# Performance work log

Measured on AMD Instinct MI355X. Metric: run time of the kernel, lower is better.

## Reference

```python
import jax, jax.numpy as jnp
import numpy as np

HEADS1, HID1 = 4, 64   # layer 1: concat -> 256
HEADS2, HID2 = 1, 64   # layer 2: out_channels
NEG_SLOPE = 0.2


def gat_layer(x_src, x_dst, W_src, W_dst, att_src, att_dst, bias, src, dst, n_tgt, heads, hid):
    # bipartite GATConv (PyG math), concat heads
    xs = (x_src @ W_src).reshape(-1, heads, hid)          # [Ns,H,C]
    xd = (x_dst @ W_dst).reshape(-1, heads, hid)          # [Nt,H,C]
    a_s = jnp.sum(xs * att_src, axis=-1)                  # [Ns,H]
    a_d = jnp.sum(xd * att_dst, axis=-1)                  # [Nt,H]
    e = jax.nn.leaky_relu(a_s[src] + a_d[dst], NEG_SLOPE) # [E,H]
    m = jax.ops.segment_max(e, dst, num_segments=n_tgt)
    m = jnp.where(jnp.isfinite(m), m, 0.0)
    ex = jnp.exp(e - m[dst])
    denom = jax.ops.segment_sum(ex, dst, num_segments=n_tgt)
    alpha = ex / (denom[dst] + 1e-16)                     # edge softmax per target
    msg = xs[src] * alpha[:, :, None]                     # [E,H,C]
    out = jax.ops.segment_sum(msg, dst, num_segments=n_tgt)
    return out.reshape(n_tgt, heads * hid) + bias


def setup_inputs() -> dict:
    key = jax.random.key(0)
    ks = jax.random.split(key, 20)
    N0, NT1, NT2 = 100000, 25000, 5000
    E1, E2 = 400000, 100000
    IN, H1 = 256, HEADS1 * HID1  # 256
    OUT = HEADS2 * HID2          # 64
    g = lambda k, sh, fan: jax.random.normal(k, sh, jnp.float32) * (1.0 / np.sqrt(fan))
    return {
        'x': jax.random.normal(ks[0], (N0, IN), jnp.float32),
        'src1': jax.random.randint(ks[1], (E1,), 0, N0),
        'dst1': jax.random.randint(ks[2], (E1,), 0, NT1),
        'src2': jax.random.randint(ks[3], (E2,), 0, NT1),
        'dst2': jax.random.randint(ks[4], (E2,), 0, NT2),
        'n_tgt1': NT1, 'n_tgt2': NT2,
        'W1_src': g(ks[5], (IN, H1), IN), 'W1_dst': g(ks[6], (IN, H1), IN),
        'att1_src': g(ks[7], (HEADS1, HID1), HID1), 'att1_dst': g(ks[8], (HEADS1, HID1), HID1),
        'bias1': jnp.zeros((H1,), jnp.float32),
        'skip1_W': g(ks[9], (IN, H1), IN), 'skip1_b': jnp.zeros((H1,), jnp.float32),
        'W2_src': g(ks[10], (H1, OUT), H1), 'W2_dst': g(ks[11], (H1, OUT), H1),
        'att2_src': g(ks[12], (HEADS2, HID2), HID2), 'att2_dst': g(ks[13], (HEADS2, HID2), HID2),
        'bias2': jnp.zeros((OUT,), jnp.float32),
        'skip2_W': g(ks[14], (H1, OUT), H1), 'skip2_b': jnp.zeros((OUT,), jnp.float32),
    }


def reference(x, src1, dst1, src2, dst2, n_tgt1, n_tgt2,
              W1_src, W1_dst, att1_src, att1_dst, bias1, skip1_W, skip1_b,
              W2_src, W2_dst, att2_src, att2_dst, bias2, skip2_W, skip2_b):
    # layer 1: conv + skip + elu (dropout inactive in eval)
    x_t1 = x[:n_tgt1]
    h = gat_layer(x, x_t1, W1_src, W1_dst, att1_src, att1_dst, bias1,
                  src1, dst1, n_tgt1, HEADS1, HID1)
    h = h + (x_t1 @ skip1_W + skip1_b)
    h = jax.nn.elu(h)
    # layer 2 (final): conv + skip, then log_softmax
    x_t2 = h[:n_tgt2]
    o = gat_layer(h, x_t2, W2_src, W2_dst, att2_src, att2_dst, bias2,
                  src2, dst2, n_tgt2, HEADS2, HID2)
    o = o + (x_t2 @ skip2_W + skip2_b)
    return jax.nn.log_softmax(o, axis=-1)
```

## Files before the change

kernel.cpp:

```cpp
#include <hip/hip_runtime.h>
#include <hip/hip_bf16.h>

using bf16 = __hip_bfloat16;
typedef __attribute__((ext_vector_type(8))) short short8;
typedef __attribute__((ext_vector_type(4))) short short4v;
typedef __attribute__((ext_vector_type(4))) float float4v;

__device__ __forceinline__ short f2bs(float x) {
    bf16 b = __float2bfloat16(x);
    return __builtin_bit_cast(short, b);
}
__device__ __forceinline__ float bs2f(short s) {
    return __uint_as_float(((unsigned)(unsigned short)s) << 16);
}
__device__ __forceinline__ void glds16(const void* g, void* l) {
    __builtin_amdgcn_global_load_lds(
        (const __attribute__((address_space(1))) unsigned int*)g,
        (__attribute__((address_space(3))) unsigned int*)l, 16, 0, 0);
}

__global__ __launch_bounds__(512, 4) void gemm_l1(
        const float* __restrict__ A, const bf16* __restrict__ Bt,
        bf16* __restrict__ xs1, bf16* __restrict__ sk1,
        float* __restrict__ as1, float* __restrict__ ad1,
        const float* __restrict__ att_s, const float* __restrict__ att_d,
        int M, int NT) {
    __shared__ short ldsB[2][32 * 512];
    const int row0 = blockIdx.x * 128;
    const int tid = threadIdx.x;
    const int wave = tid >> 6, lane = tid & 63;
    const int quad = lane >> 4, l16 = lane & 15;

    auto stageB = [&](int y, int buf) {
#pragma unroll
        for (int i = 0; i < 4; i++) {
            int blk = wave * 4 + i;
            int cb = blk >> 3, kit = blk & 7;
            glds16(&Bt[(size_t)(y * 64 + cb * 16 + l16) * 256 + kit * 32 + quad * 8],
                   &ldsB[buf][blk * 512]);
        }
    };

    stageB(0, 0);

    const int arow_ = row0 + wave * 16 + l16;
    const int arow = arow_ < M ? arow_ : M - 1;
    const float* Ap = &A[(size_t)arow * 256 + quad * 8];
    short8 afr[8];
#pragma unroll
    for (int half = 0; half < 2; half++) {
        float4v r0[4], r1[4];
#pragma unroll
        for (int k = 0; k < 4; k++) {
            r0[k] = *(const float4v*)(Ap + (half * 4 + k) * 32);
            r1[k] = *(const float4v*)(Ap + (half * 4 + k) * 32 + 4);
        }
#pragma unroll
        for (int k = 0; k < 4; k++) {
            short8 v;
#pragma unroll
            for (int j = 0; j < 4; j++) { v[j] = f2bs(r0[k][j]); v[4 + j] = f2bs(r1[k][j]); }
            afr[half * 4 + k] = v;
        }
    }

    const int ymax = row0 < NT ? 12 : 4;
    const int rbase = row0 + wave * 16 + quad * 4;

    __syncthreads();

    for (int y = 0; y < ymax; y++) {
        const int cur = y & 1;
        if (y + 1 < ymax) stageB(y + 1, cur ^ 1);

        const float4v fz = {0.f, 0.f, 0.f, 0.f};
        float4v acc[4];
#pragma unroll
        for (int n = 0; n < 4; n++) acc[n] = fz;
#pragma unroll
        for (int kit = 0; kit < 8; kit++)
#pragma unroll
            for (int n = 0; n < 4; n++) {
                short8 bf = *(short8*)&ldsB[cur][(n * 8 + kit) * 512 + lane * 8];
                acc[n] = __builtin_amdgcn_mfma_f32_16x16x32_bf16(afr[kit], bf, acc[n], 0, 0, 0);
            }

        if (y < 8) {
            const float* attc = y < 4 ? att_s : att_d;
            const int head = y & 3;
            const int aM = y < 4 ? M : NT;
            float* aout = y < 4 ? as1 : ad1;
            float av[4];
#pragma unroll
            for (int n = 0; n < 4; n++) av[n] = attc[head * 64 + n * 16 + l16];
#pragma unroll
            for (int r = 0; r < 4; r++) {
                float t = acc[0][r] * av[0] + acc[1][r] * av[1] +
                          acc[2][r] * av[2] + acc[3][r] * av[3];
                t += __shfl_xor(t, 1, 64);
                t += __shfl_xor(t, 2, 64);
                t += __shfl_xor(t, 4, 64);
                t += __shfl_xor(t, 8, 64);
                int grow = rbase + r;
                if (l16 == 0 && grow < aM) aout[(size_t)grow * 4 + head] = t;
            }
        }
        if (y < 4) {
#pragma unroll
            for (int n = 0; n < 4; n++) {
                int col = y * 64 + n * 16 + l16;
#pragma unroll
                for (int r = 0; r < 4; r++) {
                    int row = rbase + r;
                    if (row < M) xs1[(size_t)row * 256 + col] = __float2bfloat16(acc[n][r]);
                }
            }
        } else if (y >= 8) {
#pragma unroll
            for (int n = 0; n < 4; n++) {
                int scol = (y - 8) * 64 + n * 16 + l16;
#pragma unroll
                for (int r = 0; r < 4; r++) {
                    int row = rbase + r;
                    if (row < NT) sk1[(size_t)row * 256 + scol] = __float2bfloat16(acc[n][r]);
                }
            }
        }
        __syncthreads();
    }
}

__global__ __launch_bounds__(512, 4) void gemm_l2(
        const bf16* __restrict__ Ah, const bf16* __restrict__ Bt,
        float* __restrict__ x2, float* __restrict__ a2,
        const float* __restrict__ attc, int NT) {
    __shared__ short ldsB[32 * 512];
    const int y = blockIdx.y;
    const int row0 = blockIdx.x * 128;
    const int col0 = y * 64;
    const int tid = threadIdx.x;
    const int wave = tid >> 6, lane = tid & 63;
    const int quad = lane >> 4, l16 = lane & 15;

#pragma unroll
    for (int i = 0; i < 4; i++) {
        int blk = wave * 4 + i;
        int cb = blk >> 3, kit = blk & 7;
        glds16(&Bt[(size_t)(col0 + cb * 16 + l16) * 256 + kit * 32 + quad * 8],
               &ldsB[blk * 512]);
    }

    const int arow = row0 + wave * 16 + l16;
    const bf16* Ap = &Ah[(size_t)arow * 256 + quad * 8];

    short8 s[8];
#pragma unroll
    for (int kit = 0; kit < 8; kit++) s[kit] = *(const short8*)(Ap + kit * 32);

    const float4v fz = {0.f, 0.f, 0.f, 0.f};
    float4v acc[4];
#pragma unroll
    for (int n = 0; n < 4; n++) acc[n] = fz;

    __syncthreads();

#pragma unroll
    for (int kit = 0; kit < 8; kit++) {
#pragma unroll
        for (int n = 0; n < 4; n++) {
            short8 bf = *(short8*)&ldsB[(n * 8 + kit) * 512 + lane * 8];
            acc[n] = __builtin_amdgcn_mfma_f32_16x16x32_bf16(s[kit], bf, acc[n], 0, 0, 0);
        }
    }

    const int rbase = row0 + wave * 16 + quad * 4;

    if (y < 2) {
        float av[4];
#pragma unroll
        for (int n = 0; n < 4; n++) av[n] = attc[y * 64 + n * 16 + l16];
#pragma unroll
        for (int r = 0; r < 4; r++) {
            float t = acc[0][r] * av[0] + acc[1][r] * av[1] +
                      acc[2][r] * av[2] + acc[3][r] * av[3];
            t += __shfl_xor(t, 1, 64);
            t += __shfl_xor(t, 2, 64);
            t += __shfl_xor(t, 4, 64);
            t += __shfl_xor(t, 8, 64);
            int grow = rbase + r;
            if (l16 == 0 && grow < NT) a2[(size_t)grow * 2 + y] = t;
        }
    }
#pragma unroll
    for (int n = 0; n < 4; n++) {
        int col = col0 + n * 16 + l16;
#pragma unroll
        for (int r = 0; r < 4; r++) {
            int row = rbase + r;
            if (row < NT) x2[(size_t)row * 192 + col] = acc[n][r];
        }
    }
}

__global__ void prep_s(
        const int* __restrict__ s1, const int* __restrict__ d1, int E1,
        const int* __restrict__ s2, const int* __restrict__ d2, int E2,
        int* __restrict__ fill1, int* __restrict__ fill2,
        int* __restrict__ psrc1, int* __restrict__ psrc2,
        const float* __restrict__ W1s, const float* __restrict__ W1d,
        const float* __restrict__ W1sk, const float* __restrict__ W2s,
        const float* __restrict__ W2d, const float* __restrict__ W2sk,
        const float* __restrict__ a2s, const float* __restrict__ a2d,
        bf16* __restrict__ Wt1, bf16* __restrict__ Wt2,
        float* __restrict__ at2c) {
    int t = blockIdx.x * blockDim.x + threadIdx.x;
    if (t < E1) {
        int d = d1[t];
        int pos = atomicAdd(&fill1[d], 1);
        if (pos < 64) psrc1[(d << 6) + pos] = s1[t];
        return;
    }
    t -= E1;
    if (t < E2) {
        int d = d2[t];
        int pos = atomicAdd(&fill2[d], 1);
        if (pos < 64) psrc2[(d << 6) + pos] = s2[t];
        return;
    }
    t -= E2;
    if (t < 196608) {
        int n = t >> 8, k = t & 255;
        const float* W = n < 256 ? W1s : (n < 512 ? W1d : W1sk);
        Wt1[t] = __float2bfloat16(W[k * 256 + (n & 255)]);
    } else if (t < 245760) {
        int i = t - 196608;
        int n = i >> 8, k = i & 255;
        const float* W = n < 64 ? W2s : (n < 128 ? W2d : W2sk);
        Wt2[i] = __float2bfloat16(W[k * 64 + (n & 63)]);
    } else if (t < 245888) {
        int i = t - 245760;
        at2c[i] = i < 64 ? a2s[i] : a2d[i - 64];
    }
}

__global__ __launch_bounds__(256) void agg_h4(
        const int* __restrict__ fill, const int* __restrict__ psrc,
        const bf16* __restrict__ X, const float* __restrict__ as1,
        const float* __restrict__ ad1, const float* __restrict__ bias,
        const bf16* __restrict__ skip, const float* __restrict__ skipb,
        bf16* __restrict__ h) {
    __shared__ float exl[4][64][4];
    __shared__ float red[4][256];
    const int d = blockIdx.x;
    const int tid = threadIdx.x;
    const int wv = tid >> 6, lane = tid & 63;
    const int head = lane >> 4;
    int deg = fill[d];
    deg = deg < 64 ? deg : 64;
    int se = 0;
    float4v ex4 = {0.f, 0.f, 0.f, 0.f};
    const float4v ad4 = *(const float4v*)&ad1[(size_t)d * 4];
    if (lane < deg) {
        se = psrc[((size_t)d << 6) + lane];
        float4v as4 = *(const float4v*)&as1[(size_t)se * 4];
#pragma unroll
        for (int c = 0; c < 4; c++) {
            float v = as4[c] + ad4[c];
            v = v > 0.f ? v : 0.2f * v;
            ex4[c] = expf(v);
        }
    }
    *(float4v*)&exl[wv][lane][0] = ex4;
    float4v dn = ex4;
#pragma unroll
    for (int o = 32; o; o >>= 1) {
        dn.x += __shfl_xor(dn.x, o, 64);
        dn.y += __shfl_xor(dn.y, o, 64);
        dn.z += __shfl_xor(dn.z, o, 64);
        dn.w += __shfl_xor(dn.w, o, 64);
    }
    float4v acc = {0.f, 0.f, 0.f, 0.f}, acc2 = {0.f, 0.f, 0.f, 0.f};
    int p = wv;
    for (; p + 4 < deg; p += 8) {
        int sA = __shfl(se, p, 64), sB = __shfl(se, p + 4, 64);
        float aA = exl[wv][p][head], aB = exl[wv][p + 4][head];
        short4v xa = *(const short4v*)&X[(size_t)sA * 256 + lane * 4];
        short4v xb = *(const short4v*)&X[(size_t)sB * 256 + lane * 4];
        acc.x += bs2f(xa.x) * aA; acc2.x += bs2f(xb.x) * aB;
        acc.y += bs2f(xa.y) * aA; acc2.y += bs2f(xb.y) * aB;
        acc.z += bs2f(xa.z) * aA; acc2.z += bs2f(xb.z) * aB;
        acc.w += bs2f(xa.w) * aA; acc2.w += bs2f(xb.w) * aB;
    }
    for (; p < deg; p += 4) {
        int sA = __shfl(se, p, 64);
        float aA = exl[wv][p][head];
        short4v xa = *(const short4v*)&X[(size_t)sA * 256 + lane * 4];
        acc.x += bs2f(xa.x) * aA;
        acc.y += bs2f(xa.y) * aA;
        acc.z += bs2f(xa.z) * aA;
        acc.w += bs2f(xa.w) * aA;
    }
    acc.x += acc2.x; acc.y += acc2.y; acc.z += acc2.z; acc.w += acc2.w;
    *(float4v*)&red[wv][lane * 4] = acc;
    __syncthreads();
    const int f = tid;
    float sum = red[0][f] + red[1][f] + red[2][f] + red[3][f];
    int hf = f >> 6;
    float den = hf == 0 ? dn.x : hf == 1 ? dn.y : hf == 2 ? dn.z : dn.w;
    float v = sum / (den + 1e-16f) + bias[f] + __bfloat162float(skip[(size_t)d * 256 + f]) +
              skipb[f];
    h[(size_t)d * 256 + f] = __float2bfloat16(v > 0.f ? v : expm1f(v));
}

__global__ __launch_bounds__(256) void agg_h1(
        const int* __restrict__ fill2, const int* __restrict__ psrc2,
        const float* __restrict__ x2, const float* __restrict__ a2,
        const float* __restrict__ bias, const float* __restrict__ skipb,
        float* __restrict__ out, int M) {
    const int d = blockIdx.x * 4 + (threadIdx.x >> 6);
    const int lane = threadIdx.x & 63;
    if (d >= M) return;
    int deg = fill2[d];
    deg = deg < 64 ? deg : 64;
    int se = 0;
    float exv = 0.f;
    const float adv = a2[(size_t)d * 2 + 1];
    if (lane < deg) {
        se = psrc2[((size_t)d << 6) + lane];
        float v = a2[(size_t)se * 2] + adv;
        v = v > 0.f ? v : 0.2f * v;
        exv = expf(v);
    }
    float den = exv;
#pragma unroll
    for (int o = 32; o; o >>= 1) den += __shfl_xor(den, o, 64);
    float acc = 0.f, acc2 = 0.f;
    int p = 0;
    for (; p + 1 < deg; p += 2) {
        int sA = __shfl(se, p, 64), sB = __shfl(se, p + 1, 64);
        float aA = __shfl(exv, p, 64), aB = __shfl(exv, p + 1, 64);
        acc += x2[(size_t)sA * 192 + lane] * aA;
        acc2 += x2[(size_t)sB * 192 + lane] * aB;
    }
    if (p < deg) {
        int sA = __shfl(se, p, 64);
        acc += x2[(size_t)sA * 192 + lane] * __shfl(exv, p, 64);
    }
    float v = (acc + acc2) / (den + 1e-16f) + bias[lane] +
              x2[(size_t)d * 192 + 128 + lane] + skipb[lane];
    float m = v;
#pragma unroll
    for (int o = 32; o; o >>= 1) m = fmaxf(m, __shfl_xor(m, o, 64));
    float e = expf(v - m);
#pragma unroll
    for (int o = 32; o; o >>= 1) e += __shfl_xor(e, o, 64);
    out[(size_t)d * 64 + lane] = v - m - logf(e);
}

extern "C" void kernel_launch(void* const* d_in, const int* in_sizes, int n_in,
                              void* d_out, int out_size, void* d_ws, size_t ws_size,
                              hipStream_t stream) {
    const float* x        = (const float*)d_in[0];
    const int*   src1     = (const int*)d_in[1];
    const int*   dst1     = (const int*)d_in[2];
    const int*   src2     = (const int*)d_in[3];
    const int*   dst2     = (const int*)d_in[4];
    const float* W1_src   = (const float*)d_in[7];
    const float* W1_dst   = (const float*)d_in[8];
    const float* att1_src = (const float*)d_in[9];
    const float* att1_dst = (const float*)d_in[10];
    const float* bias1    = (const float*)d_in[11];
    const float* skip1_W  = (const float*)d_in[12];
    const float* skip1_b  = (const float*)d_in[13];
    const float* W2_src   = (const float*)d_in[14];
    const float* W2_dst   = (const float*)d_in[15];
    const float* att2_src = (const float*)d_in[16];
    const float* att2_dst = (const float*)d_in[17];
    const float* bias2    = (const float*)d_in[18];
    const float* skip2_b  = (const float*)d_in[20];
    const float* skip2_W  = (const float*)d_in[19];

    const int N0  = in_sizes[0] / 256;
    const int E1  = in_sizes[1];
    const int E2  = in_sizes[3];
    const int NT1 = 25000, NT2 = 5000;
    const int NT1p = 25088;

    char* ws = (char*)d_ws;
    size_t off = 0;
    auto alloc = [&](size_t b) { size_t o = off; off += (b + 255) & ~(size_t)255; return o; };
    size_t o_xs1   = alloc((size_t)N0 * 256 * 2);
    size_t o_sk1   = alloc((size_t)NT1 * 256 * 2);
    size_t o_h     = alloc((size_t)NT1p * 256 * 2);
    size_t o_as1   = alloc((size_t)N0 * 4 * 4);
    size_t o_ad1   = alloc((size_t)NT1 * 4 * 4);
    size_t o_fill  = alloc((size_t)(NT1 + NT2) * 4);
    size_t o_psrc1 = alloc((size_t)NT1 * 64 * 4);
    size_t o_psrc2 = alloc((size_t)NT2 * 64 * 4);
    size_t o_wt1   = alloc((size_t)768 * 256 * 2);
    size_t o_wt2   = alloc((size_t)192 * 256 * 2);
    size_t o_at2c  = alloc((size_t)128 * 4);
    size_t off2a = o_xs1;
    auto alloc2 = [&](size_t b) { size_t o = off2a; off2a += (b + 255) & ~(size_t)255; return o; };
    size_t o_x2 = alloc2((size_t)NT1 * 192 * 4);
    size_t o_a2 = alloc2((size_t)NT1 * 2 * 4);

    bf16*  xs1   = (bf16*)(ws + o_xs1);
    bf16*  sk1   = (bf16*)(ws + o_sk1);
    bf16*  h     = (bf16*)(ws + o_h);
    float* as1   = (float*)(ws + o_as1);
    float* ad1   = (float*)(ws + o_ad1);
    int*   fill1 = (int*)(ws + o_fill);
    int*   fill2 = fill1 + NT1;
    int*   psrc1 = (int*)(ws + o_psrc1);
    int*   psrc2 = (int*)(ws + o_psrc2);
    bf16*  Wt1   = (bf16*)(ws + o_wt1);
    bf16*  Wt2   = (bf16*)(ws + o_wt2);
    float* at2c  = (float*)(ws + o_at2c);
    float* x2    = (float*)(ws + o_x2);
    float* a2    = (float*)(ws + o_a2);

    hipMemsetAsync(fill1, 0, (size_t)(NT1 + NT2) * 4, stream);
    {
        int total = E1 + E2 + 245888;
        prep_s<<<(total + 255) / 256, 256, 0, stream>>>(
            src1, dst1, E1, src2, dst2, E2, fill1, fill2, psrc1, psrc2,
            W1_src, W1_dst, skip1_W, W2_src, W2_dst, skip2_W,
            att2_src, att2_dst, Wt1, Wt2, at2c);
    }
    gemm_l1<<<(N0 + 127) / 128, 512, 0, stream>>>(
        x, Wt1, xs1, sk1, as1, ad1, att1_src, att1_dst, N0, NT1);
    agg_h4<<<NT1, 256, 0, stream>>>(fill1, psrc1, xs1, as1, ad1, bias1, sk1, skip1_b, h);
    gemm_l2<<<dim3((NT1 + 127) / 128, 3), 512, 0, stream>>>(h, Wt2, x2, a2, at2c, NT1);
    agg_h1<<<(NT2 + 3) / 4, 256, 0, stream>>>(fill2, psrc2, x2, a2, bias2, skip2_b,
                                              (float*)d_out, NT2);
}
```

Measured before the change: 326.4 us.

## Retile layer-1 GEMM to 4 waves with two row tiles per wave

The layer-1 projection GEMM now runs 256 threads per block, and each wave owns 32 rows (two 16-row MFMA tiles) instead of 16. Each LDS B fragment is therefore reused across two MFMAs. The 64-column output step is split into two 32-column half-stages with a smaller double-buffered LDS tile. The fp32 A loads are software-pipelined against their bf16 conversion. The aim is to cut LDS traffic per MFMA and overlap global A loads, at the cost of more registers per thread and twice as many barriers per block.

```diff
diff --git a/kernel.cpp b/kernel.cpp
--- a/kernel.cpp
+++ b/kernel.cpp
@@ -19,111 +19,151 @@
         (__attribute__((address_space(3))) unsigned int*)l, 16, 0, 0);
 }
 
-__global__ __launch_bounds__(512, 4) void gemm_l1(
+__global__ __launch_bounds__(256, 4) void gemm_l1(
         const float* __restrict__ A, const bf16* __restrict__ Bt,
         bf16* __restrict__ xs1, bf16* __restrict__ sk1,
         float* __restrict__ as1, float* __restrict__ ad1,
         const float* __restrict__ att_s, const float* __restrict__ att_d,
         int M, int NT) {
-    __shared__ short ldsB[2][32 * 512];
+    __shared__ short ldsB[2][16 * 512];
     const int row0 = blockIdx.x * 128;
     const int tid = threadIdx.x;
     const int wave = tid >> 6, lane = tid & 63;
     const int quad = lane >> 4, l16 = lane & 15;
-
-    auto stageB = [&](int y, int buf) {
+    const int ymax = row0 < NT ? 12 : 4;
+    const int Hmax = 2 * ymax;
+
+    auto stageH = [&](int H, int buf) {
 #pragma unroll
         for (int i = 0; i < 4; i++) {
             int blk = wave * 4 + i;
             int cb = blk >> 3, kit = blk & 7;
-            glds16(&Bt[(size_t)(y * 64 + cb * 16 + l16) * 256 + kit * 32 + quad * 8],
+            glds16(&Bt[(size_t)(H * 32 + cb * 16 + l16) * 256 + kit * 32 + quad * 8],
                    &ldsB[buf][blk * 512]);
         }
     };
-
-    stageB(0, 0);
-
-    const int arow_ = row0 + wave * 16 + l16;
-    const int arow = arow_ < M ? arow_ : M - 1;
-    const float* Ap = &A[(size_t)arow * 256 + quad * 8];
-    short8 afr[8];
-#pragma unroll
-    for (int half = 0; half < 2; half++) {
-        float4v r0[4], r1[4];
-#pragma unroll
-        for (int k = 0; k < 4; k++) {
-            r0[k] = *(const float4v*)(Ap + (half * 4 + k) * 32);
-            r1[k] = *(const float4v*)(Ap + (half * 4 + k) * 32 + 4);
-        }
-#pragma unroll
-        for (int k = 0; k < 4; k++) {
-            short8 v;
-#pragma unroll
-            for (int j = 0; j < 4; j++) { v[j] = f2bs(r0[k][j]); v[4 + j] = f2bs(r1[k][j]); }
-            afr[half * 4 + k] = v;
-        }
-    }
-
-    const int ymax = row0 < NT ? 12 : 4;
-    const int rbase = row0 + wave * 16 + quad * 4;
-
+    stageH(0, 0);
+
+    short8 afr[2][8];
+    {
+        int r0_ = row0 + wave * 32 + l16;
+        int r1_ = r0_ + 16;
+        const int r0 = r0_ < M ? r0_ : M - 1;
+        const int r1 = r1_ < M ? r1_ : M - 1;
+        const float* Ap0 = &A[(size_t)r0 * 256 + quad * 8];
+        const float* Ap1 = &A[(size_t)r1 * 256 + quad * 8];
+        float4v pA[4], pB[4];
+        auto issue = [&](int b, float4v* pf) {
+            const float* p = (b >> 2 ? Ap1 : Ap0) + (b & 3) * 64;
+            pf[0] = *(const float4v*)(p);
+            pf[1] = *(const float4v*)(p + 4);
+            pf[2] = *(const float4v*)(p + 32);
+            pf[3] = *(const float4v*)(p + 36);
+        };
+        auto cvt = [&](int b, float4v* pf) {
+            const int m = b >> 2, k0 = (b & 3) * 2;
+            short8 v0, v1;
+#pragma unroll
+            for (int j = 0; j < 4; j++) {
+                v0[j] = f2bs(pf[0][j]); v0[4 + j] = f2bs(pf[1][j]);
+                v1[j] = f2bs(pf[2][j]); v1[4 + j] = f2bs(pf[3][j]);
+            }
+            afr[m][k0] = v0; afr[m][k0 + 1] = v1;
+        };
+        issue(0, pA);
+#pragma unroll
+        for (int b = 0; b < 7; b++) {
+            if (b & 1) { issue(b + 1, pA); cvt(b, pB); }
+            else       { issue(b + 1, pB); cvt(b, pA); }
+        }
+        cvt(7, pB);
+    }
+
+    const int rbase = row0 + wave * 32 + quad * 4;
     __syncthreads();
 
-    for (int y = 0; y < ymax; y++) {
-        const int cur = y & 1;
-        if (y + 1 < ymax) stageB(y + 1, cur ^ 1);
-
-        const float4v fz = {0.f, 0.f, 0.f, 0.f};
-        float4v acc[4];
-#pragma unroll
-        for (int n = 0; n < 4; n++) acc[n] = fz;
-#pragma unroll
-        for (int kit = 0; kit < 8; kit++)
-#pragma unroll
-            for (int n = 0; n < 4; n++) {
-                short8 bf = *(short8*)&ldsB[cur][(n * 8 + kit) * 512 + lane * 8];
-                acc[n] = __builtin_amdgcn_mfma_f32_16x16x32_bf16(afr[kit], bf, acc[n], 0, 0, 0);
+    float4v acc[2][4];
+    for (int H = 0; H < Hmax; H++) {
+        const int buf = H & 1;
+        if (H + 1 < Hmax) stageH(H + 1, buf ^ 1);
+
+        if ((H & 1) == 0) {
+            const float4v fz = {0.f, 0.f, 0.f, 0.f};
+#pragma unroll
+            for (int m = 0; m < 2; m++)
+#pragma unroll
+                for (int n = 0; n < 4; n++) acc[m][n] = fz;
+#pragma unroll
+            for (int kit = 0; kit < 8; kit++)
+#pragma unroll
+                for (int nf = 0; nf < 2; nf++) {
+                    short8 bf = *(short8*)&ldsB[buf][(nf * 8 + kit) * 512 + lane * 8];
+#pragma unroll
+                    for (int m = 0; m < 2; m++)
+                        acc[m][nf] = __builtin_amdgcn_mfma_f32_16x16x32_bf16(
+                            afr[m][kit], bf, acc[m][nf], 0, 0, 0);
+                }
+        } else {
+#pragma unroll
+            for (int kit = 0; kit < 8; kit++)
+#pragma unroll
+                for (int nf = 0; nf < 2; nf++) {
+                    short8 bf = *(short8*)&ldsB[buf][(nf * 8 + kit) * 512 + lane * 8];
+#pragma unroll
+                    for (int m = 0; m < 2; m++)
+                        acc[m][2 + nf] = __builtin_amdgcn_mfma_f32_16x16x32_bf16(
+                            afr[m][kit], bf, acc[m][2 + nf], 0, 0, 0);
+                }
+
+            const int y = H >> 1;
+            if (y < 8) {
+                const float* attc = y < 4 ? att_s : att_d;
+                const int head = y & 3;
+                const int aM = y < 4 ? M : NT;
+                float* aout = y < 4 ? as1 : ad1;
+                float av[4];
+#pragma unroll
+                for (int n = 0; n < 4; n++) av[n] = attc[head * 64 + n * 16 + l16];
+#pragma unroll
+                for (int m = 0; m < 2; m++)
+#pragma unroll
+                    for (int r = 0; r < 4; r++) {
+                        float t = acc[m][0][r] * av[0] + acc[m][1][r] * av[1] +
+                                  acc[m][2][r] * av[2] + acc[m][3][r] * av[3];
+                        t += __shfl_xor(t, 1, 64);
+                        t += __shfl_xor(t, 2, 64);
+                        t += __shfl_xor(t, 4, 64);
+                        t += __shfl_xor(t, 8, 64);
+                        int grow = rbase + m * 16 + r;
+                        if (l16 == 0 && grow < aM) aout[(size_t)grow * 4 + head] = t;
+                    }
             }
-
-        if (y < 8) {
-            const float* attc = y < 4 ? att_s : att_d;
-            const int head = y & 3;
-            const int aM = y < 4 ? M : NT;
-            float* aout = y < 4 ? as1 : ad1;
-            float av[4];
-#pragma unroll
-            for (int n = 0; n < 4; n++) av[n] = attc[head * 64 + n * 16 + l16];
-#pragma unroll
-            for (int r = 0; r < 4; r++) {
-                float t = acc[0][r] * av[0] + acc[1][r] * av[1] +
-                          acc[2][r] * av[2] + acc[3][r] * av[3];
-                t += __shfl_xor(t, 1, 64);
-                t += __shfl_xor(t, 2, 64);
-                t += __shfl_xor(t, 4, 64);
-                t += __shfl_xor(t, 8, 64);
-                int grow = rbase + r;
-                if (l16 == 0 && grow < aM) aout[(size_t)grow * 4 + head] = t;
-            }
-        }
-        if (y < 4) {
-#pragma unroll
-            for (int n = 0; n < 4; n++) {
-                int col = y * 64 + n * 16 + l16;
-#pragma unroll
-                for (int r = 0; r < 4; r++) {
-                    int row = rbase + r;
-                    if (row < M) xs1[(size_t)row * 256 + col] = __float2bfloat16(acc[n][r]);
-                }
-            }
-        } else if (y >= 8) {
-#pragma unroll
-            for (int n = 0; n < 4; n++) {
-                int scol = (y - 8) * 64 + n * 16 + l16;
-#pragma unroll
-                for (int r = 0; r < 4; r++) {
-                    int row = rbase + r;
-                    if (row < NT) sk1[(size_t)row * 256 + scol] = __float2bfloat16(acc[n][r]);
-                }
+            if (y < 4) {
+#pragma unroll
+                for (int m = 0; m < 2; m++)
+#pragma unroll
+                    for (int n = 0; n < 4; n++) {
+                        int col = y * 64 + n * 16 + l16;
+#pragma unroll
+                        for (int r = 0; r < 4; r++) {
+                            int row = rbase + m * 16 + r;
+                            if (row < M)
+                                xs1[(size_t)row * 256 + col] = __float2bfloat16(acc[m][n][r]);
+                        }
+                    }
+            } else if (y >= 8) {
+#pragma unroll
+                for (int m = 0; m < 2; m++)
+#pragma unroll
+                    for (int n = 0; n < 4; n++) {
+                        int scol = (y - 8) * 64 + n * 16 + l16;
+#pragma unroll
+                        for (int r = 0; r < 4; r++) {
+                            int row = rbase + m * 16 + r;
+                            if (row < NT)
+                                sk1[(size_t)row * 256 + scol] = __float2bfloat16(acc[m][n][r]);
+                        }
+                    }
             }
         }
         __syncthreads();
@@ -377,8 +417,8 @@
     const float* att2_src = (const float*)d_in[16];
     const float* att2_dst = (const float*)d_in[17];
     const float* bias2    = (const float*)d_in[18];
+    const float* skip2_W  = (const float*)d_in[19];
     const float* skip2_b  = (const float*)d_in[20];
-    const float* skip2_W  = (const float*)d_in[19];
 
     const int N0  = in_sizes[0] / 256;
     const int E1  = in_sizes[1];
@@ -428,7 +468,7 @@
             W1_src, W1_dst, skip1_W, W2_src, W2_dst, skip2_W,
             att2_src, att2_dst, Wt1, Wt2, at2c);
     }
-    gemm_l1<<<(N0 + 127) / 128, 512, 0, stream>>>(
+    gemm_l1<<<(N0 + 127) / 128, 256, 0, stream>>>(
         x, Wt1, xs1, sk1, as1, ad1, att1_src, att1_dst, N0, NT1);
     agg_h4<<<NT1, 256, 0, stream>>>(fill1, psrc1, xs1, as1, ad1, bias1, sk1, skip1_b, h);
     gemm_l2<<<dim3((NT1 + 127) / 128, 3), 512, 0, stream>>>(h, Wt2, x2, a2, at2c, NT1);
```

New measurement: 379.6 us. 1.16x slower.
